# Performance work log

Measured on AMD Instinct MI355X. Metric: run time of the kernel, lower is better.

The kernel has to match this reference:

```python
import jax, jax.numpy as jnp
import numpy as np
from jax import lax

DN = ('NCHW', 'OIHW', 'NCHW')

def conv(x, w, b, stride=1, pad=0):
    y = lax.conv_general_dilated(x, w, (stride, stride), ((pad, pad), (pad, pad)), dimension_numbers=DN)
    return y + b[None, :, None, None]

def conv_transpose(x, w, b):
    # torch ConvTranspose2d(k=4, s=2, p=1): w is (in_ch, out_ch, 4, 4)
    wf = jnp.flip(w, (2, 3)).transpose(1, 0, 2, 3)  # -> (out_ch, in_ch, 4, 4)
    pad = 4 - 1 - 1  # k - 1 - p = 2
    y = lax.conv_general_dilated(x, wf, (1, 1), ((pad, pad), (pad, pad)), lhs_dilation=(2, 2), dimension_numbers=DN)
    return y + b[None, :, None, None]

def setup_inputs() -> dict:
    key = jax.random.key(0)
    ks = jax.random.split(key, 16)
    HID, ZC, K = 256, 64, 512
    def w(k, shape):
        return (jax.random.normal(k, shape, jnp.float32) * 0.02)
    z = lambda n: jnp.zeros((n,), jnp.float32)
    return {
        'x': jax.random.uniform(ks[0], (8, 3, 128, 128), jnp.float32),
        'c1_w': w(ks[1], (HID, 3, 4, 4)), 'c1_b': z(HID),
        'c2_w': w(ks[2], (HID, HID, 4, 4)), 'c2_b': z(HID),
        'r0_w3': w(ks[3], (HID, HID, 3, 3)), 'r0_b3': z(HID),
        'r0_w1': w(ks[4], (HID, HID, 1, 1)), 'r0_b1': z(HID),
        'r1_w3': w(ks[5], (HID, HID, 3, 3)), 'r1_b3': z(HID),
        'r1_w1': w(ks[6], (HID, HID, 1, 1)), 'r1_b1': z(HID),
        'to_z_w': w(ks[7], (ZC, HID, 1, 1)), 'to_z_b': z(ZC),
        'codebook': jax.random.uniform(ks[8], (K, ZC), jnp.float32, -1.0 / K, 1.0 / K),
        'from_z_w': w(ks[9], (HID, ZC, 1, 1)), 'from_z_b': z(HID),
        't1_w': w(ks[10], (HID, HID, 4, 4)), 't1_b': z(HID),
        't2_w': w(ks[11], (HID, 3, 4, 4)), 't2_b': z(3),
    }

def _vqvae(x, c1_w, c1_b, c2_w, c2_b, r0_w3, r0_b3, r0_w1, r0_b1,
           r1_w3, r1_b3, r1_w1, r1_b1, to_z_w, to_z_b, codebook,
           from_z_w, from_z_b, t1_w, t1_b, t2_w, t2_b):
    # ---- Encoder ----
    h = jax.nn.relu(conv(x, c1_w, c1_b, stride=2, pad=1))
    h = jax.nn.relu(conv(h, c2_w, c2_b, stride=2, pad=1))
    for (w3, b3, w1, b1) in ((r0_w3, r0_b3, r0_w1, r0_b1), (r1_w3, r1_b3, r1_w1, r1_b1)):
        r = conv(jax.nn.relu(h), w3, b3, pad=1)
        r = conv(jax.nn.relu(r), w1, b1)
        h = h + r
    z_e = conv(h, to_z_w, to_z_b)  # [B, ZC, H/4, W/4]
    # ---- Vector quantization ----
    B, C, H, W = z_e.shape
    z_flat = z_e.transpose(0, 2, 3, 1).reshape(-1, C)  # [N, C]
    dist = (jnp.sum(z_flat * z_flat, axis=1, keepdims=True)
            - 2.0 * z_flat @ codebook.T
            + jnp.sum(codebook * codebook, axis=1)[None, :])  # [N, K]
    ids = jnp.argmin(dist, axis=1)  # [N]
    e_k_flat = codebook[ids]  # [N, C]
    e_k_st_flat = z_flat + lax.stop_gradient(e_k_flat - z_flat)
    e_k = e_k_flat.reshape(B, H, W, C).transpose(0, 3, 1, 2)
    e_k_st = e_k_st_flat.reshape(B, H, W, C).transpose(0, 3, 1, 2)
    ids = ids.reshape(B, H, W)
    # ---- Decoder ----
    d = jax.nn.relu(conv(e_k_st, from_z_w, from_z_b))
    d = jax.nn.relu(conv_transpose(d, t1_w, t1_b))
    out = jax.nn.sigmoid(conv_transpose(d, t2_w, t2_b))
    return out, z_e, e_k, ids

def reference(x, c1_w, c1_b, c2_w, c2_b, r0_w3, r0_b3, r0_w1, r0_b1,
              r1_w3, r1_b3, r1_w1, r1_b1, to_z_w, to_z_b, codebook,
              from_z_w, from_z_b, t1_w, t1_b, t2_w, t2_b):
    return _vqvae(x, c1_w, c1_b, c2_w, c2_b, r0_w3, r0_b3, r0_w1, r0_b1,
                  r1_w3, r1_b3, r1_w1, r1_b1, to_z_w, to_z_b, codebook,
                  from_z_w, from_z_b, t1_w, t1_b, t2_w, t2_b)
```

## Files before the change

### kernel.cpp

```cpp
#include <hip/hip_runtime.h>
#include <math.h>


typedef unsigned int uint;
typedef unsigned short ushort_t;
using short8 = __attribute__((ext_vector_type(8))) short;
using f32x4  = __attribute__((ext_vector_type(4))) float;

__device__ __attribute__((aligned(16))) ushort_t g_zpad[512];

static __device__ __forceinline__ int rfl(int x) { return __builtin_amdgcn_readfirstlane(x); }
static __device__ __forceinline__ ushort_t f2bf(float f) {
  uint u = __float_as_uint(f);
  return (ushort_t)((u + 0x7fffu + ((u >> 16) & 1u)) >> 16);
}
static __device__ __forceinline__ float bf2f(ushort_t b) {
  return __uint_as_float(((uint)b) << 16);
}
static __device__ __forceinline__ void gload16(const ushort_t* g, void* l) {
  __builtin_amdgcn_global_load_lds(
      (const __attribute__((address_space(1))) void*)g,
      (__attribute__((address_space(3))) void*)l, 16, 0, 0);
}

__global__ void k_transpose_w(const float* __restrict__ w, float* __restrict__ wT, int CO, int CIKK) {
  int idx = blockIdx.x * 256 + threadIdx.x;
  if (idx >= CO * CIKK) return;
  int co = idx % CO, i = idx / CO;
  wT[idx] = w[co * CIKK + i];
}

template<int KIND>
__global__ void k_prep_enc(const float* __restrict__ w, ushort_t* __restrict__ wp, int total) {
  int idx = blockIdx.x * 256 + threadIdx.x;
  if (idx >= total) return;
  int k = idx & 31, row = (idx >> 5) & 63, pl = (idx >> 11) & 1, coT = (idx >> 12) & 3, chunk = idx >> 14;
  int tap = chunk >> 3, cg = chunk & 7;
  int co = coT * 64 + row, ci = cg * 32 + k;
  int ky, kx, KK, KW;
  if (KIND == 0)      { ky = tap >> 2; kx = tap & 3;       KK = 16; KW = 4; }
  else if (KIND == 1) { ky = tap / 3;  kx = tap - ky * 3;  KK = 9;  KW = 3; }
  else                { ky = 0;        kx = 0;             KK = 1;  KW = 1; }
  float v = w[(co * 256 + ci) * KK + ky * KW + kx];
  ushort_t b0 = f2bf(v);
  wp[idx] = pl ? f2bf(v - bf2f(b0)) : b0;
}

__global__ void k_prep_t1w(const float* __restrict__ w, ushort_t* __restrict__ wb) {
  int idx = blockIdx.x * 256 + threadIdx.x;
  int kk  = idx & 31;
  int co  = (idx >> 5) & 255;
  int c8  = (idx >> 13) & 7;
  int tap = (idx >> 16) & 3;
  int par = idx >> 18;
  int ry = par & 1, rx = (par >> 1) & 1;
  int a = tap >> 1, b = tap & 1;
  int ky = ((ry + 1) & 1) + 2 * a;
  int kx = ((rx + 1) & 1) + 2 * b;
  int ci = c8 * 32 + kk;
  wb[idx] = f2bf(w[((ci * 256 + co) << 4) + ky * 4 + kx]);
}

__global__ void k_prep_t2w(const float* __restrict__ w, ushort_t* __restrict__ wb) {
  int idx = blockIdx.x * 256 + threadIdx.x;
  int k = idx & 31, co = (idx >> 5) & 15, chunk = (idx >> 9) & 31, par = idx >> 14;
  int tap = chunk >> 3, cg = chunk & 7;
  int a = tap >> 1, b = tap & 1;
  int ry = par & 1, rx = (par >> 1) & 1;
  int ky = ((ry + 1) & 1) + 2 * a;
  int kx = ((rx + 1) & 1) + 2 * b;
  int ci = cg * 32 + k;
  float v = (co < 3) ? w[((ci * 3 + co) << 4) + ky * 4 + kx] : 0.f;
  wb[idx] = f2bf(v);
}

__global__ void k_prep_cb(const float* __restrict__ cb, float* __restrict__ cnorm) {
  int idx = blockIdx.x * 256 + threadIdx.x;
  if (idx < 512) {
    float s = 0.f;
    for (int c = 0; c < 64; ++c) { float v = cb[idx * 64 + c]; s = fmaf(v, v, s); }
    cnorm[idx] = s;
  }
}

__global__ __launch_bounds__(256) void k_conv1_split(
    const float* __restrict__ in, ushort_t* __restrict__ o0, ushort_t* __restrict__ o1,
    const float* __restrict__ wT, const float* __restrict__ bias)
{
  __shared__ float s_in[3 * 360];
  const int tid = threadIdx.x;
  const int lane = tid & 63;
  const int wv = rfl(tid >> 6);
  const int px = lane & 7, py = lane >> 3;
  const int tx = blockIdx.x & 7, ty = blockIdx.x >> 3;
  const int X = tx * 8, Y = ty * 8;
  const int cob = blockIdx.y * 64 + wv * 16;
  const int n = blockIdx.z;
  float acc[16];
#pragma unroll
  for (int i = 0; i < 16; ++i) acc[i] = bias[cob + i];
  const float* inN = in + (size_t)n * 3 * 16384;
  for (int e = tid; e < 3 * 360; e += 256) {
    int col2 = e % 20; int t = e / 20; int row = t % 18; int ci = t / 18;
    int pr = col2 / 10, hc = col2 % 10, ixl = 2 * hc + pr;
    int iy = 2 * Y - 1 + row, ix = 2 * X - 1 + ixl;
    float v = 0.f;
    if (ixl < 18 && (unsigned)iy < 128u && (unsigned)ix < 128u)
      v = inN[ci * 16384 + iy * 128 + ix];
    s_in[e] = v;
  }
  __syncthreads();
  const float* wc = wT + cob;
#pragma unroll
  for (int c = 0; c < 3; ++c) {
    const float* base = s_in + c * 360 + py * 40 + px;
#pragma unroll
    for (int ky = 0; ky < 4; ++ky) {
#pragma unroll
      for (int kx = 0; kx < 4; ++kx) {
        float iv = base[ky * 20 + (kx & 1) * 10 + (kx >> 1)];
        const float* w = wc + (size_t)(c * 16 + ky * 4 + kx) * 256;
#pragma unroll
        for (int i = 0; i < 16; ++i) acc[i] = fmaf(iv, w[i], acc[i]);
      }
    }
  }
  const int pxg = n * 4096 + (Y + py) * 64 + (X + px);
  uint p0[8], p1[8];
#pragma unroll
  for (int i = 0; i < 8; ++i) {
    float va = fmaxf(acc[2 * i], 0.f), vb = fmaxf(acc[2 * i + 1], 0.f);
    ushort_t a0 = f2bf(va), b0 = f2bf(vb);
    ushort_t a1 = f2bf(va - bf2f(a0)), b1 = f2bf(vb - bf2f(b0));
    p0[i] = (uint)a0 | ((uint)b0 << 16);
    p1[i] = (uint)a1 | ((uint)b1 << 16);
  }
  ushort_t* d0 = o0 + (size_t)pxg * 256 + cob;
  ushort_t* d1 = o1 + (size_t)pxg * 256 + cob;
  uint4 v0a; v0a.x = p0[0]; v0a.y = p0[1]; v0a.z = p0[2]; v0a.w = p0[3];
  uint4 v0b; v0b.x = p0[4]; v0b.y = p0[5]; v0b.z = p0[6]; v0b.w = p0[7];
  uint4 v1a; v1a.x = p1[0]; v1a.y = p1[1]; v1a.z = p1[2]; v1a.w = p1[3];
  uint4 v1b; v1b.x = p1[4]; v1b.y = p1[5]; v1b.z = p1[6]; v1b.w = p1[7];
  *(uint4*)d0 = v0a; *(uint4*)(d0 + 8) = v0b;
  *(uint4*)d1 = v1a; *(uint4*)(d1 + 8) = v1b;
}

template<int KIND>
__global__ __launch_bounds__(256) void k_enc_mfma_split(
    const ushort_t* __restrict__ x0, const ushort_t* __restrict__ x1,
    const ushort_t* __restrict__ wp, float* __restrict__ part)
{
  __shared__ ushort_t smem[2][12288];
  const int tid = threadIdx.x, lane = tid & 63, wv = tid >> 6;
  const int l15 = lane & 15, q = lane >> 4;
  const int pxT = blockIdx.x, coT = blockIdx.y;
  constexpr int NCH = (KIND == 0) ? 128 : 72;
  const int CH0 = blockIdx.z * (NCH / 2), CH1 = CH0 + NCH / 2;
  f32x4 acc[4][2];
#pragma unroll
  for (int m = 0; m < 4; ++m)
#pragma unroll
    for (int n = 0; n < 2; ++n) acc[m][n] = (f32x4){0.f, 0.f, 0.f, 0.f};

  const int r0 = tid >> 2, kq = tid & 3;
  int bimg[2], bu[2], bvc[2];
#pragma unroll
  for (int r = 0; r < 2; ++r) {
    int bpx = pxT * 128 + r0 + r * 64;
    bimg[r] = bpx >> 10; int bp = bpx & 1023; bu[r] = bp >> 5; bvc[r] = bp & 31;
  }
  const ushort_t* srcB[2][2];
  int ptap = -1;
  auto retap = [&](int tap) {
    ptap = tap;
    int ky, kx;
    if (KIND == 0) { ky = tap >> 2; kx = tap & 3; }
    else           { ky = tap / 3;  kx = tap - ky * 3; }
#pragma unroll
    for (int r = 0; r < 2; ++r) {
      bool v; size_t rowb;
      if (KIND == 0) {
        int iy = 2 * bu[r] - 1 + ky, ix = 2 * bvc[r] - 1 + kx;
        v = ((unsigned)iy < 64u) && ((unsigned)ix < 64u);
        rowb = ((size_t)(bimg[r] * 4096 + iy * 64 + ix)) << 8;
      } else {
        int iy = bu[r] - 1 + ky, ix = bvc[r] - 1 + kx;
        v = ((unsigned)iy < 32u) && ((unsigned)ix < 32u);
        rowb = ((size_t)(bimg[r] * 1024 + iy * 32 + ix)) << 8;
      }
      srcB[r][0] = (v ? (x0 + rowb) : g_zpad) + kq * 8;
      srcB[r][1] = (v ? (x1 + rowb) : g_zpad) + kq * 8;
    }
  };

  const int wvb = wv * 1024;
  auto stage = [&](int chunk, int bi) {
    const int tap = chunk >> 3, cg = chunk & 7;
    if (tap != ptap) retap(tap);
    char* bufb = (char*)smem[bi];
    const ushort_t* ap = wp + ((size_t)(chunk * 4 + coT) << 12) + tid * 8;
    gload16(ap,        bufb + wvb);
    gload16(ap + 2048, bufb + 4096 + wvb);
    const int ko = cg * 32;
    gload16(srcB[0][0] + ko, bufb + 8192 + wvb);
    gload16(srcB[1][0] + ko, bufb + 8192 + 4096 + wvb);
    gload16(srcB[0][1] + ko, bufb + 16384 + wvb);
    gload16(srcB[1][1] + ko, bufb + 16384 + 4096 + wvb);
  };
  auto compute = [&](const ushort_t* buf) {
    const ushort_t* sA = buf;
    const ushort_t* sB = buf + 4096;
    short8 af[4][2], bf[2][2];
#pragma unroll
    for (int m = 0; m < 4; ++m)
#pragma unroll
      for (int pl = 0; pl < 2; ++pl)
        af[m][pl] = *(const short8*)(sA + pl * 2048 + (m * 16 + l15) * 32 + q * 8);
#pragma unroll
    for (int n = 0; n < 2; ++n)
#pragma unroll
      for (int pl = 0; pl < 2; ++pl)
        bf[n][pl] = *(const short8*)(sB + pl * 4096 + (wv * 32 + n * 16 + l15) * 32 + q * 8);
#pragma unroll
    for (int m = 0; m < 4; ++m)
#pragma unroll
      for (int n = 0; n < 2; ++n) {
        acc[m][n] = __builtin_amdgcn_mfma_f32_16x16x32_bf16(af[m][0], bf[n][0], acc[m][n], 0, 0, 0);
        acc[m][n] = __builtin_amdgcn_mfma_f32_16x16x32_bf16(af[m][0], bf[n][1], acc[m][n], 0, 0, 0);
        acc[m][n] = __builtin_amdgcn_mfma_f32_16x16x32_bf16(af[m][1], bf[n][0], acc[m][n], 0, 0, 0);
      }
  };

  stage(CH0, 0);
  __syncthreads();
  int cur = 0;
  for (int c = CH0; c < CH1; ++c) {
    if (c + 1 < CH1) stage(c + 1, cur ^ 1);
    compute(smem[cur]);
    __syncthreads();
    cur ^= 1;
  }

  float* pz = part + ((size_t)blockIdx.z << 21);
#pragma unroll
  for (int m = 0; m < 4; ++m) {
#pragma unroll
    for (int n = 0; n < 2; ++n) {
#pragma unroll
      for (int r = 0; r < 4; ++r) {
        const int co_l = m * 16 + q * 4 + r;
        const int px_l = wv * 32 + n * 16 + l15;
        const int px = pxT * 128 + px_l;
        const int img = px >> 10, pp = px & 1023;
        const size_t ha = ((size_t)(img * 256 + coT * 64 + co_l)) * 1024 + pp;
        pz[ha] = acc[m][n][r];
      }
    }
  }
}

template<bool WH>
__global__ __launch_bounds__(256) void k_enc_epi(
    const float* __restrict__ part, float* __restrict__ h32,
    ushort_t* __restrict__ s0, ushort_t* __restrict__ s1,
    const float* __restrict__ bias)
{
  const int px = blockIdx.x * 256 + threadIdx.x;
  const int co0 = blockIdx.y * 16;
  const int img = px >> 10, pp = px & 1023;
  const float* part1 = part + (1u << 21);
  uint p0[8], p1[8];
#pragma unroll
  for (int i = 0; i < 8; ++i) {
    size_t ha = ((size_t)(img * 256 + co0 + 2 * i)) * 1024 + pp;
    size_t hb = ha + 1024;
    float va = part[ha] + part1[ha] + bias[co0 + 2 * i];
    float vb = part[hb] + part1[hb] + bias[co0 + 2 * i + 1];
    float sa, sb;
    if (WH) {
      va = fmaxf(va, 0.f); vb = fmaxf(vb, 0.f);
      h32[ha] = va; h32[hb] = vb; sa = va; sb = vb;
    } else { sa = fmaxf(va, 0.f); sb = fmaxf(vb, 0.f); }
    ushort_t a0 = f2bf(sa), b0 = f2bf(sb);
    p0[i] = (uint)a0 | ((uint)b0 << 16);
    p1[i] = (uint)f2bf(sa - bf2f(a0)) | ((uint)f2bf(sb - bf2f(b0)) << 16);
  }
  ushort_t* d0 = s0 + (size_t)px * 256 + co0;
  ushort_t* d1 = s1 + (size_t)px * 256 + co0;
  uint4 v0a; v0a.x = p0[0]; v0a.y = p0[1]; v0a.z = p0[2]; v0a.w = p0[3];
  uint4 v0b; v0b.x = p0[4]; v0b.y = p0[5]; v0b.z = p0[6]; v0b.w = p0[7];
  uint4 v1a; v1a.x = p1[0]; v1a.y = p1[1]; v1a.z = p1[2]; v1a.w = p1[3];
  uint4 v1b; v1b.x = p1[4]; v1b.y = p1[5]; v1b.z = p1[6]; v1b.w = p1[7];
  *(uint4*)d0 = v0a; *(uint4*)(d0 + 8) = v0b;
  *(uint4*)d1 = v1a; *(uint4*)(d1 + 8) = v1b;
}

template<bool WS>
__global__ __launch_bounds__(256) void k_enc_mfma(
    const ushort_t* __restrict__ x0, const ushort_t* __restrict__ x1,
    const ushort_t* __restrict__ wp, const float* __restrict__ bias,
    float* __restrict__ h32, ushort_t* __restrict__ sp0, ushort_t* __restrict__ sp1)
{
  __shared__ ushort_t smem[24576];
  const int tid = threadIdx.x, lane = tid & 63, wv = tid >> 6;
  const int l15 = lane & 15, q = lane >> 4;
  const int pxT = blockIdx.x, coT = blockIdx.y;
  f32x4 acc[4][2];
#pragma unroll
  for (int m = 0; m < 4; ++m)
#pragma unroll
    for (int n = 0; n < 2; ++n) acc[m][n] = (f32x4){0.f, 0.f, 0.f, 0.f};

  const int r0 = tid >> 2, kq = tid & 3;
  const ushort_t* srcB[2][2];
#pragma unroll
  for (int r = 0; r < 2; ++r) {
    size_t rowb = ((size_t)(pxT * 128 + r0 + r * 64)) << 8;
    srcB[r][0] = x0 + rowb + kq * 8;
    srcB[r][1] = x1 + rowb + kq * 8;
  }
  const int wvb = wv * 1024;
  auto stage = [&](int c, int bi) {
    char* bufb = (char*)(smem + bi * 12288);
    const ushort_t* ap = wp + ((size_t)(c * 4 + coT) << 12) + tid * 8;
    gload16(ap,        bufb + wvb);
    gload16(ap + 2048, bufb + 4096 + wvb);
    const int ko = c * 32;
    gload16(srcB[0][0] + ko, bufb + 8192 + wvb);
    gload16(srcB[1][0] + ko, bufb + 8192 + 4096 + wvb);
    gload16(srcB[0][1] + ko, bufb + 16384 + wvb);
    gload16(srcB[1][1] + ko, bufb + 16384 + 4096 + wvb);
  };
  auto compute = [&](const ushort_t* buf) {
    const ushort_t* sA = buf;
    const ushort_t* sB = buf + 4096;
    short8 af[4][2], bf[2][2];
#pragma unroll
    for (int m = 0; m < 4; ++m)
#pragma unroll
      for (int pl = 0; pl < 2; ++pl)
        af[m][pl] = *(const short8*)(sA + pl * 2048 + (m * 16 + l15) * 32 + q * 8);
#pragma unroll
    for (int n = 0; n < 2; ++n)
#pragma unroll
      for (int pl = 0; pl < 2; ++pl)
        bf[n][pl] = *(const short8*)(sB + pl * 4096 + (wv * 32 + n * 16 + l15) * 32 + q * 8);
#pragma unroll
    for (int m = 0; m < 4; ++m)
#pragma unroll
      for (int n = 0; n < 2; ++n) {
        acc[m][n] = __builtin_amdgcn_mfma_f32_16x16x32_bf16(af[m][0], bf[n][0], acc[m][n], 0, 0, 0);
        acc[m][n] = __builtin_amdgcn_mfma_f32_16x16x32_bf16(af[m][0], bf[n][1], acc[m][n], 0, 0, 0);
        acc[m][n] = __builtin_amdgcn_mfma_f32_16x16x32_bf16(af[m][1], bf[n][0], acc[m][n], 0, 0, 0);
      }
  };

  stage(0, 0);
  __syncthreads();
  int cur = 0;
  for (int c = 0; c < 8; ++c) {
    if (c + 1 < 8) stage(c + 1, cur ^ 1);
    compute(smem + cur * 12288);
    __syncthreads();
    cur ^= 1;
  }

#pragma unroll
  for (int m = 0; m < 4; ++m) {
#pragma unroll
    for (int n = 0; n < 2; ++n) {
#pragma unroll
      for (int r = 0; r < 4; ++r) {
        const int co_l = m * 16 + q * 4 + r;
        const int px_l = wv * 32 + n * 16 + l15;
        float v = acc[m][n][r] + bias[coT * 64 + co_l];
        const int px = pxT * 128 + px_l;
        const int img = px >> 10, pp = px & 1023;
        const size_t ha = ((size_t)(img * 256 + coT * 64 + co_l)) * 1024 + pp;
        v += h32[ha];
        h32[ha] = v;
        if (WS) {
          float sv = fmaxf(v, 0.f);
          ushort_t b0 = f2bf(sv);
          smem[px_l * 72 + co_l] = b0;
          smem[9216 + px_l * 72 + co_l] = f2bf(sv - bf2f(b0));
        }
      }
    }
  }
  if (WS) {
    __syncthreads();
#pragma unroll
    for (int i = 0; i < 8; ++i) {
      int idx = tid + 256 * i;
      int pl = idx >> 10, w2 = idx & 1023, pxl = w2 >> 3, g = w2 & 7;
      uint4 vv = *(const uint4*)(smem + pl * 9216 + pxl * 72 + g * 8);
      ushort_t* dst = (pl ? sp1 : sp0) + ((size_t)(pxT * 128 + pxl)) * 256 + coT * 64 + g * 8;
      *(uint4*)dst = vv;
    }
  }
}

__global__ __launch_bounds__(256) void k_conv1x1(
    const float* __restrict__ in, float* __restrict__ out,
    const float* __restrict__ wT, const float* __restrict__ bias,
    int CI, int CO, int P)
{
  const int p = blockIdx.x * 256 + threadIdx.x;
  const int cob = blockIdx.y * 16;
  const int n = blockIdx.z;
  const float* inN = in + (size_t)n * CI * P + p;
  float acc[16];
#pragma unroll
  for (int i = 0; i < 16; ++i) acc[i] = bias[cob + i];
  const float* wr = wT + cob;
#pragma unroll 4
  for (int ci = 0; ci < CI; ++ci) {
    float iv = inN[(size_t)ci * P];
    const float* w = wr + (size_t)ci * CO;
#pragma unroll
    for (int i = 0; i < 16; ++i) acc[i] = fmaf(iv, w[i], acc[i]);
  }
  float* outN = out + (size_t)n * CO * P + p;
#pragma unroll
  for (int i = 0; i < 16; ++i) outN[(size_t)(cob + i) * P] = acc[i];
}

__global__ __launch_bounds__(256) void k_vq_part(
    const float* __restrict__ z_e, const float* __restrict__ cb,
    const float* __restrict__ cnorm, float* __restrict__ pbest, int* __restrict__ pbid)
{
  int g = blockIdx.x * 256 + threadIdx.x;
  int chunk = blockIdx.y;
  int img = g >> 10, p = g & 1023;
  const float* zp = z_e + (size_t)img * 64 * 1024 + p;
  float z[64];
#pragma unroll
  for (int c = 0; c < 64; ++c) z[c] = zp[(size_t)c * 1024];
  float best = 3.4e38f; int bid = chunk << 5;
  const int j0 = chunk << 5;
  for (int j = j0; j < j0 + 32; ++j) {
    const float* cj = cb + j * 64;
    float m = 0.f;
#pragma unroll
    for (int c = 0; c < 64; ++c) m = fmaf(z[c], cj[c], m);
    float d = fmaf(-2.f, m, cnorm[j]);
    if (d < best) { best = d; bid = j; }
  }
  pbest[chunk * 8192 + g] = best;
  pbid[chunk * 8192 + g] = bid;
}

__global__ __launch_bounds__(256) void k_vq_reduce(
    const float* __restrict__ pbest, const int* __restrict__ pbid,
    const float* __restrict__ cb, float* __restrict__ ids_f, float* __restrict__ ek)
{
  int g = blockIdx.x * 256 + threadIdx.x;
  float best = 3.4e38f; int bid = 0;
#pragma unroll
  for (int ch = 0; ch < 16; ++ch) {
    float d = pbest[ch * 8192 + g];
    int b = pbid[ch * 8192 + g];
    if (d < best) { best = d; bid = b; }
  }
  ids_f[g] = (float)bid;
  int img = g >> 10, p = g & 1023;
  const float* cbid = cb + bid * 64;
  float* ekp = ek + (size_t)img * 64 * 1024 + p;
#pragma unroll
  for (int c = 0; c < 64; ++c) ekp[(size_t)c * 1024] = cbid[c];
}

__global__ __launch_bounds__(256) void k_from_z(
    const float* __restrict__ ek, ushort_t* __restrict__ nhwc,
    const float* __restrict__ wT, const float* __restrict__ bias)
{
  const int p = blockIdx.x * 256 + threadIdx.x;
  const int co0 = blockIdx.y * 16;
  const int n = blockIdx.z;
  const float* inN = ek + (size_t)n * 64 * 1024 + p;
  float acc[16];
#pragma unroll
  for (int i = 0; i < 16; ++i) acc[i] = bias[co0 + i];
#pragma unroll 4
  for (int ci = 0; ci < 64; ++ci) {
    float iv = inN[(size_t)ci * 1024];
    const float* w = wT + (size_t)ci * 256 + co0;
#pragma unroll
    for (int i = 0; i < 16; ++i) acc[i] = fmaf(iv, w[i], acc[i]);
  }
  uint pk[8];
#pragma unroll
  for (int i = 0; i < 8; ++i) {
    ushort_t lo = f2bf(fmaxf(acc[2 * i], 0.f));
    ushort_t hi = f2bf(fmaxf(acc[2 * i + 1], 0.f));
    pk[i] = (uint)lo | ((uint)hi << 16);
  }
  ushort_t* op = nhwc + (((size_t)n * 1024 + p) * 256 + co0);
  uint4 v0; v0.x = pk[0]; v0.y = pk[1]; v0.z = pk[2]; v0.w = pk[3];
  uint4 v1; v1.x = pk[4]; v1.y = pk[5]; v1.z = pk[6]; v1.w = pk[7];
  *(uint4*)(op) = v0;
  *(uint4*)(op + 8) = v1;
}

__global__ __launch_bounds__(256) void k_mfma_t1(
    const ushort_t* __restrict__ nhwc, const ushort_t* __restrict__ wb,
    const float* __restrict__ bias, ushort_t* __restrict__ t1o)
{
  __shared__ ushort_t smem[2][8192];
  const int tid = threadIdx.x;
  const int lane = tid & 63;
  const int wv = tid >> 6;
  const int wm = wv & 1, wn = wv >> 1;
  const int l15 = lane & 15, q = lane >> 4;
  const int pxT = blockIdx.x, coT = blockIdx.y, par = blockIdx.z;
  const int ry = par & 1, rx = (par >> 1) & 1;
  const int pxbase = pxT * 128;
  const int img = pxbase >> 10;
  f32x4 acc[4][4];
#pragma unroll
  for (int i = 0; i < 4; ++i)
#pragma unroll
    for (int j = 0; j < 4; ++j) acc[i][j] = (f32x4){0.f, 0.f, 0.f, 0.f};

  const int srow = tid >> 2, kg = tid & 3;
  int bu2[2], bv2[2];
#pragma unroll
  for (int r = 0; r < 2; ++r) {
    int px = pxbase + srow + r * 64;
    bu2[r] = (px >> 5) & 31; bv2[r] = px & 31;
  }
  const ushort_t* nb[2];
  int ptap = -1;
  auto retap = [&](int tap) {
    ptap = tap;
    int ta = tap >> 1, tb = tap & 1;
#pragma unroll
    for (int r = 0; r < 2; ++r) {
      int iy = bu2[r] + ry - ta, ix = bv2[r] + rx - tb;
      bool v = ((unsigned)iy < 32u) && ((unsigned)ix < 32u);
      nb[r] = (v ? (nhwc + (((size_t)(img * 1024 + iy * 32 + ix)) << 8)) : g_zpad) + kg * 8;
    }
  };
  const int wvb = wv * 1024;
  auto stage = [&](int c, int bi) {
    const int tap = c >> 3, c8 = c & 7;
    if (tap != ptap) retap(tap);
    char* bufb = (char*)smem[bi];
    const ushort_t* Abase = wb + ((size_t)((par * 4 + tap) * 8 + c8) << 13) + coT * 4096 + tid * 8;
    gload16(Abase,        bufb + wvb);
    gload16(Abase + 2048, bufb + 4096 + wvb);
    const int ko = c8 * 32;
    gload16(nb[0] + ko, bufb + 8192 + wvb);
    gload16(nb[1] + ko, bufb + 8192 + 4096 + wvb);
  };
  auto compute = [&](const ushort_t* buf) {
    const ushort_t* sA = buf;
    const ushort_t* sB = buf + 4096;
    short8 af[4], bfr[4];
#pragma unroll
    for (int i = 0; i < 4; ++i)
      af[i] = *(const short8*)(sA + (wm * 64 + i * 16 + l15) * 32 + q * 8);
#pragma unroll
    for (int j = 0; j < 4; ++j)
      bfr[j] = *(const short8*)(sB + (wn * 64 + j * 16 + l15) * 32 + q * 8);
#pragma unroll
    for (int i = 0; i < 4; ++i)
#pragma unroll
      for (int j = 0; j < 4; ++j)
        acc[i][j] = __builtin_amdgcn_mfma_f32_16x16x32_bf16(af[i], bfr[j], acc[i][j], 0, 0, 0);
  };

  stage(0, 0);
  __syncthreads();
  int cur = 0;
  for (int c = 0; c < 32; ++c) {
    if (c + 1 < 32) stage(c + 1, cur ^ 1);
    compute(smem[cur]);
    __syncthreads();
    cur ^= 1;
  }

#pragma unroll
  for (int i = 0; i < 4; ++i) {
    int co = coT * 128 + wm * 64 + i * 16 + q * 4;
#pragma unroll
    for (int j = 0; j < 4; ++j) {
      int px = pxbase + wn * 64 + j * 16 + l15;
      int u = (px >> 5) & 31, vv = px & 31;
      int oy = 2 * u + ry, ox = 2 * vv + rx;
      ushort_t e0 = f2bf(fmaxf(acc[i][j][0] + bias[co + 0], 0.f));
      ushort_t e1 = f2bf(fmaxf(acc[i][j][1] + bias[co + 1], 0.f));
      ushort_t e2 = f2bf(fmaxf(acc[i][j][2] + bias[co + 2], 0.f));
      ushort_t e3 = f2bf(fmaxf(acc[i][j][3] + bias[co + 3], 0.f));
      uint2 pk; pk.x = (uint)e0 | ((uint)e1 << 16); pk.y = (uint)e2 | ((uint)e3 << 16);
      *(uint2*)(t1o + ((size_t)(img * 4096 + oy * 64 + ox) * 256 + co)) = pk;
    }
  }
}

__global__ __launch_bounds__(256) void k_mfma_t2(
    const ushort_t* __restrict__ t1o, const ushort_t* __restrict__ wb,
    const float* __restrict__ bias, float* __restrict__ out)
{
  __shared__ ushort_t sA2[256 * 32];
  __shared__ ushort_t sB2[16 * 32];
  const int tid = threadIdx.x, lane = tid & 63, wv = tid >> 6;
  const int l15 = lane & 15, q = lane >> 4;
  const int pxb = blockIdx.x * 256;
  const int par = blockIdx.y;
  const int ry = par & 1, rx = (par >> 1) & 1;
  f32x4 acc[4];
#pragma unroll
  for (int m = 0; m < 4; ++m) acc[m] = (f32x4){0.f, 0.f, 0.f, 0.f};
  const int kg = tid & 3;
  const int ssw = ((tid >> 2) & 7) << 3;
  size_t rb[4]; bool rv[4];
  for (int chunk = 0; chunk < 32; ++chunk) {
    const int tap = chunk >> 3, cg = chunk & 7;
    const int a = tap >> 1, b = tap & 1;
    if ((chunk & 7) == 0) {
#pragma unroll
      for (int i = 0; i < 4; ++i) {
        int row = (tid >> 2) + 64 * i;
        int px = pxb + row;
        int img = px >> 12, p = px & 4095, u = p >> 6, v = p & 63;
        int iy = u + ry - a, ix = v + rx - b;
        rv[i] = ((unsigned)iy < 64u) && ((unsigned)ix < 64u);
        rb[i] = ((size_t)(img * 4096 + iy * 64 + ix)) << 8;
      }
    }
    uint4 av[4];
#pragma unroll
    for (int i = 0; i < 4; ++i) {
      if (rv[i]) av[i] = *(const uint4*)(t1o + rb[i] + cg * 32 + kg * 8);
      else { av[i].x = 0; av[i].y = 0; av[i].z = 0; av[i].w = 0; }
    }
    uint4 bv;
    if (tid < 64) bv = *(const uint4*)(wb + ((size_t)(par * 32 + chunk)) * 512 + tid * 8);
    __syncthreads();
#pragma unroll
    for (int i = 0; i < 4; ++i)
      *(uint4*)(sA2 + (((((tid >> 2) + 64 * i) * 32) + kg * 8) ^ ssw)) = av[i];
    if (tid < 64) *(uint4*)(sB2 + ((tid * 8) ^ ssw)) = bv;
    __syncthreads();
    short8 bf = *(const short8*)(sB2 + ((l15 * 32 + q * 8) ^ ((l15 & 7) << 3)));
#pragma unroll
    for (int m = 0; m < 4; ++m) {
      const int row = wv * 64 + m * 16 + l15;
      short8 af = *(const short8*)(sA2 + ((row * 32 + q * 8) ^ ((row & 7) << 3)));
      acc[m] = __builtin_amdgcn_mfma_f32_16x16x32_bf16(af, bf, acc[m], 0, 0, 0);
    }
    __syncthreads();
  }
  const int co = l15;
  if (co < 3) {
    float bco = bias[co];
#pragma unroll
    for (int m = 0; m < 4; ++m) {
#pragma unroll
      for (int r = 0; r < 4; ++r) {
        int px = pxb + wv * 64 + m * 16 + q * 4 + r;
        int img = px >> 12, p = px & 4095, u = p >> 6, v = p & 63;
        size_t addr = ((size_t)(img * 3 + co)) * 16384 + (2 * u + ry) * 128 + (2 * v + rx);
        out[addr] = 1.f / (1.f + expf(-(acc[m][r] + bco)));
      }
    }
  }
}

extern "C" void kernel_launch(void* const* d_in, const int* in_sizes, int n_in,
                              void* d_out, int out_size, void* d_ws, size_t ws_size,
                              hipStream_t stream) {
  (void)in_sizes; (void)n_in; (void)out_size; (void)ws_size;
  const float* x      = (const float*)d_in[0];
  const float* c1_w   = (const float*)d_in[1];
  const float* c1_b   = (const float*)d_in[2];
  const float* c2_w   = (const float*)d_in[3];
  const float* c2_b   = (const float*)d_in[4];
  const float* r0_w3  = (const float*)d_in[5];
  const float* r0_b3  = (const float*)d_in[6];
  const float* r0_w1  = (const float*)d_in[7];
  const float* r0_b1  = (const float*)d_in[8];
  const float* r1_w3  = (const float*)d_in[9];
  const float* r1_b3  = (const float*)d_in[10];
  const float* r1_w1  = (const float*)d_in[11];
  const float* r1_b1  = (const float*)d_in[12];
  const float* to_z_w = (const float*)d_in[13];
  const float* to_z_b = (const float*)d_in[14];
  const float* cb     = (const float*)d_in[15];
  const float* from_z_w = (const float*)d_in[16];
  const float* from_z_b = (const float*)d_in[17];
  const float* t1_w   = (const float*)d_in[18];
  const float* t1_b   = (const float*)d_in[19];
  const float* t2_w   = (const float*)d_in[20];
  const float* t2_b   = (const float*)d_in[21];

  float* wsf = (float*)d_ws;
  ushort_t* xs1p0 = (ushort_t*)(wsf + 0);
  ushort_t* xs1p1 = (ushort_t*)(wsf + 4194304);
  float*    cp0   = wsf + 8388608;
  float*    h32   = wsf + 8388608;
  float*    qp0   = wsf + 4194304;
  ushort_t* sE0   = (ushort_t*)(wsf + 0);
  ushort_t* sE1   = (ushort_t*)(wsf + 1048576);
  ushort_t* sF0   = (ushort_t*)(wsf + 2097152);
  ushort_t* sF1   = (ushort_t*)(wsf + 3145728);
  float*    pbest = wsf + 0;
  int*      pbid  = (int*)(wsf + 131072);
  ushort_t* t1out = (ushort_t*)(wsf + 2097152);
  ushort_t* decn  = (ushort_t*)(wsf + 6291456);
  ushort_t* wp_c2   = (ushort_t*)(wsf + 12582912);
  ushort_t* wp_r0w3 = (ushort_t*)(wsf + 13631488);
  ushort_t* wp_r1w3 = (ushort_t*)(wsf + 14221312);
  ushort_t* wp_r0w1 = (ushort_t*)(wsf + 14811136);
  ushort_t* wp_r1w1 = (ushort_t*)(wsf + 14876672);
  float*    wt_c1   = wsf + 14942208;
  float*    wt_toz  = wsf + 14954496;
  float*    wt_fromz= wsf + 14970880;
  ushort_t* t1wb    = (ushort_t*)(wsf + 14987264);
  ushort_t* w2pk    = (ushort_t*)(wsf + 15511552);
  float*    cnorm   = wsf + 15544320;

  float* out_img = (float*)d_out;
  float* z_e_out = out_img + 393216;
  float* e_k_out = z_e_out + 524288;
  float* ids_out = e_k_out + 524288;

  k_transpose_w<<<48, 256, 0, stream>>>(c1_w, wt_c1, 256, 48);
  k_transpose_w<<<64, 256, 0, stream>>>(to_z_w, wt_toz, 64, 256);
  k_transpose_w<<<64, 256, 0, stream>>>(from_z_w, wt_fromz, 256, 64);
  k_prep_enc<0><<<8192, 256, 0, stream>>>(c2_w,  wp_c2,   128 << 14);
  k_prep_enc<1><<<4608, 256, 0, stream>>>(r0_w3, wp_r0w3, 72 << 14);
  k_prep_enc<1><<<4608, 256, 0, stream>>>(r1_w3, wp_r1w3, 72 << 14);
  k_prep_enc<2><<<512,  256, 0, stream>>>(r0_w1, wp_r0w1, 8 << 14);
  k_prep_enc<2><<<512,  256, 0, stream>>>(r1_w1, wp_r1w1, 8 << 14);
  k_prep_t1w<<<4096, 256, 0, stream>>>(t1_w, t1wb);
  k_prep_t2w<<<256, 256, 0, stream>>>(t2_w, w2pk);
  k_prep_cb<<<2, 256, 0, stream>>>(cb, cnorm);

  k_conv1_split<<<dim3(64, 4, 8), 256, 0, stream>>>(x, xs1p0, xs1p1, wt_c1, c1_b);
  k_enc_mfma_split<0><<<dim3(64, 4, 2), 256, 0, stream>>>(xs1p0, xs1p1, wp_c2, cp0);
  k_enc_epi<true><<<dim3(32, 16), 256, 0, stream>>>(cp0, h32, sE0, sE1, c2_b);
  k_enc_mfma_split<1><<<dim3(64, 4, 2), 256, 0, stream>>>(sE0, sE1, wp_r0w3, qp0);
  k_enc_epi<false><<<dim3(32, 16), 256, 0, stream>>>(qp0, nullptr, sE0, sE1, r0_b3);
  k_enc_mfma<true ><<<dim3(64, 4), 256, 0, stream>>>(
      sE0, sE1, wp_r0w1, r0_b1, h32, sF0, sF1);
  k_enc_mfma_split<1><<<dim3(64, 4, 2), 256, 0, stream>>>(sF0, sF1, wp_r1w3, qp0);
  k_enc_epi<false><<<dim3(32, 16), 256, 0, stream>>>(qp0, nullptr, sE0, sE1, r1_b3);
  k_enc_mfma<false><<<dim3(64, 4), 256, 0, stream>>>(
      sE0, sE1, wp_r1w1, r1_b1, h32, nullptr, nullptr);
  k_conv1x1<<<dim3(4, 4, 8), 256, 0, stream>>>(h32, z_e_out, wt_toz, to_z_b, 256, 64, 1024);

  k_vq_part<<<dim3(32, 16), 256, 0, stream>>>(z_e_out, cb, cnorm, pbest, pbid);
  k_vq_reduce<<<32, 256, 0, stream>>>(pbest, pbid, cb, ids_out, e_k_out);

  k_from_z<<<dim3(4, 16, 8), 256, 0, stream>>>(e_k_out, decn, wt_fromz, from_z_b);
  k_mfma_t1<<<dim3(64, 2, 4), 256, 0, stream>>>(decn, t1wb, t1_b, t1out);
  k_mfma_t2<<<dim3(128, 4), 256, 0, stream>>>(t1out, w2pk, t2_b, out_img);
}
```

Before: 433.9 us.

## Load MFMA weight fragments directly to registers and add halo-tiled 3x3 conv kernel

```diff
diff --git a/kernel.cpp b/kernel.cpp
--- a/kernel.cpp
+++ b/kernel.cpp
@@ -145,17 +145,15 @@
   *(uint4*)d1 = v1a; *(uint4*)(d1 + 8) = v1b;
 }
 
-template<int KIND>
 __global__ __launch_bounds__(256) void k_enc_mfma_split(
     const ushort_t* __restrict__ x0, const ushort_t* __restrict__ x1,
     const ushort_t* __restrict__ wp, float* __restrict__ part)
 {
-  __shared__ ushort_t smem[2][12288];
+  __shared__ ushort_t smem[2][8192];
   const int tid = threadIdx.x, lane = tid & 63, wv = tid >> 6;
   const int l15 = lane & 15, q = lane >> 4;
   const int pxT = blockIdx.x, coT = blockIdx.y;
-  constexpr int NCH = (KIND == 0) ? 128 : 72;
-  const int CH0 = blockIdx.z * (NCH / 2), CH1 = CH0 + NCH / 2;
+  const int CH0 = blockIdx.z * 64, CH1 = CH0 + 64;
   f32x4 acc[4][2];
 #pragma unroll
   for (int m = 0; m < 4; ++m)
@@ -173,21 +171,12 @@
   int ptap = -1;
   auto retap = [&](int tap) {
     ptap = tap;
-    int ky, kx;
-    if (KIND == 0) { ky = tap >> 2; kx = tap & 3; }
-    else           { ky = tap / 3;  kx = tap - ky * 3; }
+    int ky = tap >> 2, kx = tap & 3;
 #pragma unroll
     for (int r = 0; r < 2; ++r) {
-      bool v; size_t rowb;
-      if (KIND == 0) {
-        int iy = 2 * bu[r] - 1 + ky, ix = 2 * bvc[r] - 1 + kx;
-        v = ((unsigned)iy < 64u) && ((unsigned)ix < 64u);
-        rowb = ((size_t)(bimg[r] * 4096 + iy * 64 + ix)) << 8;
-      } else {
-        int iy = bu[r] - 1 + ky, ix = bvc[r] - 1 + kx;
-        v = ((unsigned)iy < 32u) && ((unsigned)ix < 32u);
-        rowb = ((size_t)(bimg[r] * 1024 + iy * 32 + ix)) << 8;
-      }
+      int iy = 2 * bu[r] - 1 + ky, ix = 2 * bvc[r] - 1 + kx;
+      bool v = ((unsigned)iy < 64u) && ((unsigned)ix < 64u);
+      size_t rowb = ((size_t)(bimg[r] * 4096 + iy * 64 + ix)) << 8;
       srcB[r][0] = (v ? (x0 + rowb) : g_zpad) + kq * 8;
       srcB[r][1] = (v ? (x1 + rowb) : g_zpad) + kq * 8;
     }
@@ -198,29 +187,28 @@
     const int tap = chunk >> 3, cg = chunk & 7;
     if (tap != ptap) retap(tap);
     char* bufb = (char*)smem[bi];
-    const ushort_t* ap = wp + ((size_t)(chunk * 4 + coT) << 12) + tid * 8;
-    gload16(ap,        bufb + wvb);
-    gload16(ap + 2048, bufb + 4096 + wvb);
     const int ko = cg * 32;
-    gload16(srcB[0][0] + ko, bufb + 8192 + wvb);
-    gload16(srcB[1][0] + ko, bufb + 8192 + 4096 + wvb);
-    gload16(srcB[0][1] + ko, bufb + 16384 + wvb);
-    gload16(srcB[1][1] + ko, bufb + 16384 + 4096 + wvb);
-  };
-  auto compute = [&](const ushort_t* buf) {
-    const ushort_t* sA = buf;
-    const ushort_t* sB = buf + 4096;
-    short8 af[4][2], bf[2][2];
-#pragma unroll
-    for (int m = 0; m < 4; ++m)
+    gload16(srcB[0][0] + ko, bufb + wvb);
+    gload16(srcB[1][0] + ko, bufb + 4096 + wvb);
+    gload16(srcB[0][1] + ko, bufb + 8192 + wvb);
+    gload16(srcB[1][1] + ko, bufb + 12288 + wvb);
+  };
+  const ushort_t* wpl = wp + l15 * 32 + q * 8 + ((size_t)coT << 12);
+  auto loadA = [&](int chunk, short8 (&af)[4][2]) {
+    const ushort_t* ap = wpl + ((size_t)chunk << 14);
+#pragma unroll
+    for (int m = 0; m < 4; ++m) {
+      af[m][0] = *(const short8*)(ap + m * 512);
+      af[m][1] = *(const short8*)(ap + 2048 + m * 512);
+    }
+  };
+  auto compute = [&](short8 (&af)[4][2], const ushort_t* buf) {
+    short8 bf[2][2];
+#pragma unroll
+    for (int n = 0; n < 2; ++n)
 #pragma unroll
       for (int pl = 0; pl < 2; ++pl)
-        af[m][pl] = *(const short8*)(sA + pl * 2048 + (m * 16 + l15) * 32 + q * 8);
-#pragma unroll
-    for (int n = 0; n < 2; ++n)
-#pragma unroll
-      for (int pl = 0; pl < 2; ++pl)
-        bf[n][pl] = *(const short8*)(sB + pl * 4096 + (wv * 32 + n * 16 + l15) * 32 + q * 8);
+        bf[n][pl] = *(const short8*)(buf + pl * 4096 + (wv * 32 + n * 16 + l15) * 32 + q * 8);
 #pragma unroll
     for (int m = 0; m < 4; ++m)
 #pragma unroll
@@ -231,12 +219,19 @@
       }
   };
 
+  short8 afC[4][2], afN[4][2];
   stage(CH0, 0);
+  loadA(CH0, afC);
   __syncthreads();
   int cur = 0;
-  for (int c = CH0; c < CH1; ++c) {
-    if (c + 1 < CH1) stage(c + 1, cur ^ 1);
-    compute(smem[cur]);
+  for (int c = CH0; c < CH1; c += 2) {
+    stage(c + 1, cur ^ 1);
+    loadA(c + 1, afN);
+    compute(afC, smem[cur]);
+    __syncthreads();
+    cur ^= 1;
+    if (c + 2 < CH1) { stage(c + 2, cur ^ 1); loadA(c + 2, afC); }
+    compute(afN, smem[cur]);
     __syncthreads();
     cur ^= 1;
   }
@@ -253,6 +248,102 @@
         const int px = pxT * 128 + px_l;
         const int img = px >> 10, pp = px & 1023;
         const size_t ha = ((size_t)(img * 256 + coT * 64 + co_l)) * 1024 + pp;
+        pz[ha] = acc[m][n][r];
+      }
+    }
+  }
+}
+
+__global__ __launch_bounds__(256) void k_enc_mfma_3x3(
+    const ushort_t* __restrict__ x0, const ushort_t* __restrict__ x1,
+    const ushort_t* __restrict__ wp, float* __restrict__ part)
+{
+  __shared__ ushort_t smem[2][14336];
+  const int tid = threadIdx.x, lane = tid & 63, wv = tid >> 6;
+  const int l15 = lane & 15, q = lane >> 4;
+  const int pxT = blockIdx.x, coT = blockIdx.y;
+  const int CG0 = blockIdx.z * 4, CG1 = CG0 + 4;
+  const int img = pxT >> 3;
+  const int U0 = (pxT & 7) * 4;
+  f32x4 acc[4][2];
+#pragma unroll
+  for (int m = 0; m < 4; ++m)
+#pragma unroll
+    for (int n = 0; n < 2; ++n) acc[m][n] = (f32x4){0.f, 0.f, 0.f, 0.f};
+
+  const ushort_t* srcp[7];
+#pragma unroll
+  for (int i = 0; i < 7; ++i) {
+    int slot = i * 256 + tid;
+    int pl = slot >= 816 ? 1 : 0;
+    int rem = slot - pl * 816;
+    int rr = rem / 136;
+    int c4 = rem - rr * 136;
+    int cc = c4 >> 2, kq2 = c4 & 3;
+    int iy = U0 - 1 + rr, ix = cc - 1;
+    bool valid = (slot < 1632) && ((unsigned)iy < 32u) && ((unsigned)ix < 32u);
+    const ushort_t* base = valid
+        ? ((pl ? x1 : x0) + (((size_t)(img * 1024 + iy * 32 + ix)) << 8))
+        : g_zpad;
+    srcp[i] = base + kq2 * 8;
+  }
+  const int wvb = wv * 1024;
+  auto stageH = [&](int cg, int bi) {
+    char* bufb = (char*)smem[bi];
+    const int ko = cg * 32;
+#pragma unroll
+    for (int i = 0; i < 7; ++i) gload16(srcp[i] + ko, bufb + i * 4096 + wvb);
+  };
+  const ushort_t* wpl = wp + l15 * 32 + q * 8 + ((size_t)coT << 12);
+
+  stageH(CG0, 0);
+  __syncthreads();
+  int cur = 0;
+  for (int cg = CG0; cg < CG1; ++cg) {
+    if (cg + 1 < CG1) stageH(cg + 1, cur ^ 1);
+    const ushort_t* buf = smem[cur];
+#pragma unroll 3
+    for (int tap = 0; tap < 9; ++tap) {
+      const int ky = tap / 3, kx = tap - ky * 3;
+      const int chunk = tap * 8 + cg;
+      const ushort_t* ap = wpl + ((size_t)chunk << 14);
+      short8 af[4][2], bf[2][2];
+#pragma unroll
+      for (int m = 0; m < 4; ++m) {
+        af[m][0] = *(const short8*)(ap + m * 512);
+        af[m][1] = *(const short8*)(ap + 2048 + m * 512);
+      }
+      const int r = wv + ky;
+#pragma unroll
+      for (int n = 0; n < 2; ++n)
+#pragma unroll
+        for (int pl = 0; pl < 2; ++pl)
+          bf[n][pl] = *(const short8*)(buf + pl * 6528 + r * 1088 + (n * 16 + l15 + kx) * 32 + q * 8);
+#pragma unroll
+      for (int m = 0; m < 4; ++m)
+#pragma unroll
+        for (int n = 0; n < 2; ++n) {
+          acc[m][n] = __builtin_amdgcn_mfma_f32_16x16x32_bf16(af[m][0], bf[n][0], acc[m][n], 0, 0, 0);
+          acc[m][n] = __builtin_amdgcn_mfma_f32_16x16x32_bf16(af[m][0], bf[n][1], acc[m][n], 0, 0, 0);
+          acc[m][n] = __builtin_amdgcn_mfma_f32_16x16x32_bf16(af[m][1], bf[n][0], acc[m][n], 0, 0, 0);
+        }
+    }
+    __syncthreads();
+    cur ^= 1;
+  }
+
+  float* pz = part + ((size_t)blockIdx.z << 21);
+#pragma unroll
+  for (int m = 0; m < 4; ++m) {
+#pragma unroll
+    for (int n = 0; n < 2; ++n) {
+#pragma unroll
+      for (int r = 0; r < 4; ++r) {
+        const int co_l = m * 16 + q * 4 + r;
+        const int px_l = wv * 32 + n * 16 + l15;
+        const int px = pxT * 128 + px_l;
+        const int imgp = px >> 10, pp = px & 1023;
+        const size_t ha = ((size_t)(imgp * 256 + coT * 64 + co_l)) * 1024 + pp;
         pz[ha] = acc[m][n][r];
       }
     }
@@ -301,7 +392,7 @@
     const ushort_t* __restrict__ wp, const float* __restrict__ bias,
     float* __restrict__ h32, ushort_t* __restrict__ sp0, ushort_t* __restrict__ sp1)
 {
-  __shared__ ushort_t smem[24576];
+  __shared__ ushort_t smem[18432];
   const int tid = threadIdx.x, lane = tid & 63, wv = tid >> 6;
   const int l15 = lane & 15, q = lane >> 4;
   const int pxT = blockIdx.x, coT = blockIdx.y;
@@ -321,30 +412,29 @@
   }
   const int wvb = wv * 1024;
   auto stage = [&](int c, int bi) {
-    char* bufb = (char*)(smem + bi * 12288);
-    const ushort_t* ap = wp + ((size_t)(c * 4 + coT) << 12) + tid * 8;
-    gload16(ap,        bufb + wvb);
-    gload16(ap + 2048, bufb + 4096 + wvb);
+    char* bufb = (char*)(smem + bi * 8192);
     const int ko = c * 32;
-    gload16(srcB[0][0] + ko, bufb + 8192 + wvb);
-    gload16(srcB[1][0] + ko, bufb + 8192 + 4096 + wvb);
-    gload16(srcB[0][1] + ko, bufb + 16384 + wvb);
-    gload16(srcB[1][1] + ko, bufb + 16384 + 4096 + wvb);
-  };
-  auto compute = [&](const ushort_t* buf) {
-    const ushort_t* sA = buf;
-    const ushort_t* sB = buf + 4096;
-    short8 af[4][2], bf[2][2];
-#pragma unroll
-    for (int m = 0; m < 4; ++m)
+    gload16(srcB[0][0] + ko, bufb + wvb);
+    gload16(srcB[1][0] + ko, bufb + 4096 + wvb);
+    gload16(srcB[0][1] + ko, bufb + 8192 + wvb);
+    gload16(srcB[1][1] + ko, bufb + 12288 + wvb);
+  };
+  const ushort_t* wpl = wp + l15 * 32 + q * 8 + ((size_t)coT << 12);
+  auto loadA = [&](int c, short8 (&af)[4][2]) {
+    const ushort_t* ap = wpl + ((size_t)c << 14);
+#pragma unroll
+    for (int m = 0; m < 4; ++m) {
+      af[m][0] = *(const short8*)(ap + m * 512);
+      af[m][1] = *(const short8*)(ap + 2048 + m * 512);
+    }
+  };
+  auto compute = [&](short8 (&af)[4][2], const ushort_t* buf) {
+    short8 bf[2][2];
+#pragma unroll
+    for (int n = 0; n < 2; ++n)
 #pragma unroll
       for (int pl = 0; pl < 2; ++pl)
-        af[m][pl] = *(const short8*)(sA + pl * 2048 + (m * 16 + l15) * 32 + q * 8);
-#pragma unroll
-    for (int n = 0; n < 2; ++n)
-#pragma unroll
-      for (int pl = 0; pl < 2; ++pl)
-        bf[n][pl] = *(const short8*)(sB + pl * 4096 + (wv * 32 + n * 16 + l15) * 32 + q * 8);
+        bf[n][pl] = *(const short8*)(buf + pl * 4096 + (wv * 32 + n * 16 + l15) * 32 + q * 8);
 #pragma unroll
     for (int m = 0; m < 4; ++m)
 #pragma unroll
@@ -355,12 +445,19 @@
       }
   };
 
+  short8 afC[4][2], afN[4][2];
   stage(0, 0);
+  loadA(0, afC);
   __syncthreads();
   int cur = 0;
-  for (int c = 0; c < 8; ++c) {
-    if (c + 1 < 8) stage(c + 1, cur ^ 1);
-    compute(smem + cur * 12288);
+  for (int c = 0; c < 8; c += 2) {
+    stage(c + 1, cur ^ 1);
+    loadA(c + 1, afN);
+    compute(afC, smem + cur * 8192);
+    __syncthreads();
+    cur ^= 1;
+    if (c + 2 < 8) { stage(c + 2, cur ^ 1); loadA(c + 2, afC); }
+    compute(afN, smem + cur * 8192);
     __syncthreads();
     cur ^= 1;
   }
@@ -507,7 +604,7 @@
     const ushort_t* __restrict__ nhwc, const ushort_t* __restrict__ wb,
     const float* __restrict__ bias, ushort_t* __restrict__ t1o)
 {
-  __shared__ ushort_t smem[2][8192];
+  __shared__ ushort_t smem[2][4096];
   const int tid = threadIdx.x;
   const int lane = tid & 63;
   const int wv = tid >> 6;
@@ -547,23 +644,22 @@
     const int tap = c >> 3, c8 = c & 7;
     if (tap != ptap) retap(tap);
     char* bufb = (char*)smem[bi];
-    const ushort_t* Abase = wb + ((size_t)((par * 4 + tap) * 8 + c8) << 13) + coT * 4096 + tid * 8;
-    gload16(Abase,        bufb + wvb);
-    gload16(Abase + 2048, bufb + 4096 + wvb);
     const int ko = c8 * 32;
-    gload16(nb[0] + ko, bufb + 8192 + wvb);
-    gload16(nb[1] + ko, bufb + 8192 + 4096 + wvb);
-  };
-  auto compute = [&](const ushort_t* buf) {
-    const ushort_t* sA = buf;
-    const ushort_t* sB = buf + 4096;
-    short8 af[4], bfr[4];
-#pragma unroll
-    for (int i = 0; i < 4; ++i)
-      af[i] = *(const short8*)(sA + (wm * 64 + i * 16 + l15) * 32 + q * 8);
+    gload16(nb[0] + ko, bufb + wvb);
+    gload16(nb[1] + ko, bufb + 4096 + wvb);
+  };
+  const ushort_t* wA = wb + coT * 4096 + (wm * 64 + l15) * 32 + q * 8;
+  auto loadA = [&](int c, short8 (&af)[4]) {
+    const int tap = c >> 3, c8 = c & 7;
+    const ushort_t* ap = wA + ((size_t)((par * 4 + tap) * 8 + c8) << 13);
+#pragma unroll
+    for (int i = 0; i < 4; ++i) af[i] = *(const short8*)(ap + i * 512);
+  };
+  auto compute = [&](short8 (&af)[4], const ushort_t* buf) {
+    short8 bfr[4];
 #pragma unroll
     for (int j = 0; j < 4; ++j)
-      bfr[j] = *(const short8*)(sB + (wn * 64 + j * 16 + l15) * 32 + q * 8);
+      bfr[j] = *(const short8*)(buf + (wn * 64 + j * 16 + l15) * 32 + q * 8);
 #pragma unroll
     for (int i = 0; i < 4; ++i)
 #pragma unroll
@@ -571,12 +667,19 @@
         acc[i][j] = __builtin_amdgcn_mfma_f32_16x16x32_bf16(af[i], bfr[j], acc[i][j], 0, 0, 0);
   };
 
+  short8 afC[4], afN[4];
   stage(0, 0);
+  loadA(0, afC);
   __syncthreads();
   int cur = 0;
-  for (int c = 0; c < 32; ++c) {
-    if (c + 1 < 32) stage(c + 1, cur ^ 1);
-    compute(smem[cur]);
+  for (int c = 0; c < 32; c += 2) {
+    stage(c + 1, cur ^ 1);
+    loadA(c + 1, afN);
+    compute(afC, smem[cur]);
+    __syncthreads();
+    cur ^= 1;
+    if (c + 2 < 32) { stage(c + 2, cur ^ 1); loadA(c + 2, afC); }
+    compute(afN, smem[cur]);
     __syncthreads();
     cur ^= 1;
   }
@@ -740,13 +843,13 @@
   k_prep_cb<<<2, 256, 0, stream>>>(cb, cnorm);
 
   k_conv1_split<<<dim3(64, 4, 8), 256, 0, stream>>>(x, xs1p0, xs1p1, wt_c1, c1_b);
-  k_enc_mfma_split<0><<<dim3(64, 4, 2), 256, 0, stream>>>(xs1p0, xs1p1, wp_c2, cp0);
+  k_enc_mfma_split<<<dim3(64, 4, 2), 256, 0, stream>>>(xs1p0, xs1p1, wp_c2, cp0);
   k_enc_epi<true><<<dim3(32, 16), 256, 0, stream>>>(cp0, h32, sE0, sE1, c2_b);
-  k_enc_mfma_split<1><<<dim3(64, 4, 2), 256, 0, stream>>>(sE0, sE1, wp_r0w3, qp0);
+  k_enc_mfma_3x3<<<dim3(64, 4, 2), 256, 0, stream>>>(sE0, sE1, wp_r0w3, qp0);
   k_enc_epi<false><<<dim3(32, 16), 256, 0, stream>>>(qp0, nullptr, sE0, sE1, r0_b3);
   k_enc_mfma<true ><<<dim3(64, 4), 256, 0, stream>>>(
       sE0, sE1, wp_r0w1, r0_b1, h32, sF0, sF1);
-  k_enc_mfma_split<1><<<dim3(64, 4, 2), 256, 0, stream>>>(sF0, sF1, wp_r1w3, qp0);
+  k_enc_mfma_3x3<<<dim3(64, 4, 2), 256, 0, stream>>>(sF0, sF1, wp_r1w3, qp0);
   k_enc_epi<false><<<dim3(32, 16), 256, 0, stream>>>(qp0, nullptr, sE0, sE1, r1_b3);
   k_enc_mfma<false><<<dim3(64, 4), 256, 0, stream>>>(
       sE0, sE1, wp_r1w1, r1_b1, h32, nullptr, nullptr);
```

Result: slower. 501.8 us (+15.6%).
